# Kernel tuning notes

Measured on AMD Instinct MI355X. Metric: run time of the kernel, lower is better.

The kernel has to match this reference:

```python
import jax, jax.numpy as jnp
import numpy as np

B, T, C = 2, 2048, 2048
N_HEAD, N_KV = 16, 4
HD = C // N_HEAD          # 128
ROPE_THETA = 10000.0


def setup_inputs() -> dict:
    key = jax.random.key(0)
    ks = jax.random.split(key, 6)
    std = 0.02
    x = jax.random.normal(ks[0], (B, T, C), dtype=jnp.float32)
    Wq = jax.random.normal(ks[1], (C, C), dtype=jnp.float32) * std
    Wk = jax.random.normal(ks[2], (C, N_KV * HD), dtype=jnp.float32) * std
    Wv = jax.random.normal(ks[3], (C, N_KV * HD), dtype=jnp.float32) * std
    Wo = jax.random.normal(ks[4], (C, C), dtype=jnp.float32) * std
    # real RoPE frequencies: freqs_cis = exp(i * t * theta^{-2j/hd})
    inv_freq = 1.0 / (ROPE_THETA ** (jnp.arange(0, HD, 2, dtype=jnp.float32) / HD))
    ang = jnp.arange(T, dtype=jnp.float32)[:, None] * inv_freq[None, :]  # [T, HD//2]
    return {"x": x, "Wq": Wq, "Wk": Wk, "Wv": Wv, "Wo": Wo,
            "freqs_cos": jnp.cos(ang), "freqs_sin": jnp.sin(ang)}


def _rope(t, cos, sin):
    # t: [B, H, T, HD]; cos/sin: [T, HD//2] -> complex rotate even/odd pairs
    tr = t.reshape(*t.shape[:-1], HD // 2, 2)
    re, im = tr[..., 0], tr[..., 1]
    c = cos[None, None, :, :]
    s = sin[None, None, :, :]
    out = jnp.stack([re * c - im * s, re * s + im * c], axis=-1)
    return out.reshape(t.shape)


def reference(x, Wq, Wk, Wv, Wo, freqs_cos, freqs_sin):
    Bm, Tm, Cm = x.shape
    q = (x @ Wq).reshape(Bm, Tm, N_HEAD, HD).transpose(0, 2, 1, 3)  # [B,H,T,HD]
    k = (x @ Wk).reshape(Bm, Tm, N_KV, HD).transpose(0, 2, 1, 3)    # [B,Hkv,T,HD]
    v = (x @ Wv).reshape(Bm, Tm, N_KV, HD).transpose(0, 2, 1, 3)
    q = _rope(q, freqs_cos, freqs_sin)
    k = _rope(k, freqs_cos, freqs_sin)
    rep = N_HEAD // N_KV
    k = jnp.repeat(k, rep, axis=1)  # GQA repeat_kv -> [B,H,T,HD]
    v = jnp.repeat(v, rep, axis=1)
    scale = 1.0 / jnp.sqrt(jnp.asarray(HD, dtype=x.dtype))
    att = jnp.einsum("bhqd,bhkd->bhqk", q, k) * scale
    causal = jnp.tril(jnp.ones((Tm, Tm), dtype=bool))
    att = jnp.where(causal[None, None], att, jnp.asarray(-jnp.inf, att.dtype))
    att = jax.nn.softmax(att, axis=-1)
    y = jnp.einsum("bhqk,bhkd->bhqd", att, v)
    y = y.transpose(0, 2, 1, 3).reshape(Bm, Tm, Cm)
    return y @ Wo
```

## Files before the change

kernel.cpp:

```cpp
#include <hip/hip_runtime.h>

#define B_ 2
#define T_ 2048
#define C_ 2048
#define NH_ 16
#define NKV_ 4
#define HD_ 128
#define REP_ (NH_ / NKV_)
#define LDQKV 3072

typedef unsigned short u16;
typedef __bf16 bf16x8v __attribute__((ext_vector_type(8)));
typedef float f32x4v __attribute__((ext_vector_type(4)));

__device__ __forceinline__ u16 f2bf(float f) {
    unsigned int u;
    __builtin_memcpy(&u, &f, 4);
    u += 0x7FFFu + ((u >> 16) & 1u);
    return (u16)(u >> 16);
}
__device__ __forceinline__ unsigned int pk2(float a, float b) {
    unsigned int ua, ub;
    __builtin_memcpy(&ua, &a, 4);
    __builtin_memcpy(&ub, &b, 4);
    ua += 0x8000u; ub += 0x8000u;
    return (ua >> 16) | (ub & 0xFFFF0000u);
}
__device__ __forceinline__ bf16x8v load8(const u16* p) {
    return *reinterpret_cast<const bf16x8v*>(p);
}
__device__ __forceinline__ void gl16(const u16* g, u16* l) {
    __builtin_amdgcn_global_load_lds(
        (const __attribute__((address_space(1))) void*)(g),
        (__attribute__((address_space(3))) void*)(l), 16, 0, 0);
}
__device__ __forceinline__ void stg(const u16* g, u16* l, int tid, int K) {
    gl16(g, l + tid * 8);
    gl16(g + (size_t)64 * K, l + 4096 + tid * 8);
}
#define BAR()      __builtin_amdgcn_s_barrier()
#define LGKM0()    asm volatile("s_waitcnt lgkmcnt(0)" ::: "memory")
#define SCHED0()   __builtin_amdgcn_sched_barrier(0)
#define PRIO(x)    __builtin_amdgcn_s_setprio(x)

__global__ void cvt_f32_bf16(const float* __restrict__ in, u16* __restrict__ out, int n4) {
    int i = blockIdx.x * blockDim.x + threadIdx.x;
    if (i >= n4) return;
    float4 v = reinterpret_cast<const float4*>(in)[i];
    ushort4 o;
    o.x = f2bf(v.x); o.y = f2bf(v.y); o.z = f2bf(v.z); o.w = f2bf(v.w);
    reinterpret_cast<ushort4*>(out)[i] = o;
}

__global__ void xpose_f32_bf16(const float* __restrict__ in, u16* __restrict__ out,
                               int R, int Cc) {
    __shared__ u16 tile[32][33];
    int bx = blockIdx.x * 32, by = blockIdx.y * 32;
    int tx = threadIdx.x, ty = threadIdx.y;
    for (int i = 0; i < 32; i += 8)
        tile[ty + i][tx] = f2bf(in[(size_t)(by + ty + i) * Cc + bx + tx]);
    __syncthreads();
    for (int i = 0; i < 32; i += 8)
        out[(size_t)(bx + ty + i) * R + by + tx] = tile[tx][ty + i];
}

__global__ __launch_bounds__(512, 2) void gemm_qkv(const u16* __restrict__ A,
                                                   const u16* __restrict__ BT,
                                                   u16* __restrict__ Cq,
                                                   u16* __restrict__ vtb,
                                                   const float* __restrict__ cb,
                                                   const float* __restrict__ sb,
                                                   int M, int N, int K) {
    __shared__ __align__(16) u16 As[2][2][8192];
    __shared__ __align__(16) u16 Bs[2][2][8192];
    int tid = threadIdx.x;
    int lane = tid & 63, wave = tid >> 6;
    int wm = wave >> 2, wn = wave & 3;
    int m15 = lane & 15, quad = lane >> 4;

    int nbx = N >> 8;
    int bid = blockIdx.x, cpx = gridDim.x >> 3;
    int swz = (bid & 7) * cpx + (bid >> 3);
    int m0 = (swz / nbx) * 256, n0 = (swz % nbx) * 256;

    const u16* gA0 = A + (size_t)(m0 + (tid >> 3)) * K + (((tid & 7) ^ ((tid >> 3) & 7)) * 8);
    const u16* gB0 = BT + (size_t)(n0 + (tid >> 3)) * K + (((tid & 7) ^ ((tid >> 3) & 7)) * 8);

    int sw8 = m15 & 7;
    int co0 = (quad ^ sw8) * 8;
    int co1 = ((4 + quad) ^ sw8) * 8;
    const u16* aB = &As[0][0][0] + wm * 8192 + m15 * 64;
    const u16* bB = &Bs[0][0][0] + (wn >> 1) * 8192 + ((wn & 1) * 64 + m15) * 64;

    f32x4v acc[8][4] = {};
    int NT = K >> 6;

    stg(gB0, &Bs[0][0][0], tid, K);
    stg(gB0 + (size_t)128 * K, &Bs[0][1][0], tid, K);
    stg(gA0, &As[0][0][0], tid, K);
    stg(gA0 + (size_t)128 * K, &As[0][1][0], tid, K);
    stg(gB0 + 64, &Bs[1][0][0], tid, K);
    stg(gB0 + (size_t)128 * K + 64, &Bs[1][1][0], tid, K);
    asm volatile("s_waitcnt vmcnt(4)" ::: "memory");
    SCHED0();
    BAR();

    for (int t = 0; t < NT; t++) {
        int d = t & 1;
        const u16* aT = aB + d * 16384;
        const u16* bT = bB + d * 16384;
        bf16x8v a0[4][2], a1[4][2], b0[2][2], b1[2][2];

#pragma unroll
        for (int mt = 0; mt < 4; mt++) {
            a0[mt][0] = load8(aT + mt * 1024 + co0);
            a0[mt][1] = load8(aT + mt * 1024 + co1);
        }
#pragma unroll
        for (int nt = 0; nt < 2; nt++) {
            b0[nt][0] = load8(bT + nt * 1024 + co0);
            b0[nt][1] = load8(bT + nt * 1024 + co1);
        }
        if (t + 1 < NT) stg(gA0 + (t + 1) * 64, &As[1 - d][0][0], tid, K);
        BAR(); LGKM0(); SCHED0(); PRIO(1);
#pragma unroll
        for (int kc = 0; kc < 2; kc++)
#pragma unroll
            for (int mt = 0; mt < 4; mt++)
#pragma unroll
                for (int nt = 0; nt < 2; nt++)
                    acc[mt][nt] = __builtin_amdgcn_mfma_f32_16x16x32_bf16(
                        a0[mt][kc], b0[nt][kc], acc[mt][nt], 0, 0, 0);
        PRIO(0); BAR();

#pragma unroll
        for (int nt = 0; nt < 2; nt++) {
            b1[nt][0] = load8(bT + (nt + 2) * 1024 + co0);
            b1[nt][1] = load8(bT + (nt + 2) * 1024 + co1);
        }
        if (t + 1 < NT) stg(gA0 + (size_t)128 * K + (t + 1) * 64, &As[1 - d][1][0], tid, K);
        BAR(); LGKM0(); SCHED0(); PRIO(1);
#pragma unroll
        for (int kc = 0; kc < 2; kc++)
#pragma unroll
            for (int mt = 0; mt < 4; mt++)
#pragma unroll
                for (int nt = 0; nt < 2; nt++)
                    acc[mt][nt + 2] = __builtin_amdgcn_mfma_f32_16x16x32_bf16(
                        a0[mt][kc], b1[nt][kc], acc[mt][nt + 2], 0, 0, 0);
        PRIO(0); BAR();

#pragma unroll
        for (int mt = 0; mt < 4; mt++) {
            a1[mt][0] = load8(aT + (mt + 4) * 1024 + co0);
            a1[mt][1] = load8(aT + (mt + 4) * 1024 + co1);
        }
        if (t + 2 < NT) stg(gB0 + (t + 2) * 64, &Bs[d][0][0], tid, K);
        BAR(); LGKM0(); SCHED0(); PRIO(1);
#pragma unroll
        for (int kc = 0; kc < 2; kc++)
#pragma unroll
            for (int mt = 0; mt < 4; mt++)
#pragma unroll
                for (int nt = 0; nt < 2; nt++)
                    acc[mt + 4][nt] = __builtin_amdgcn_mfma_f32_16x16x32_bf16(
                        a1[mt][kc], b0[nt][kc], acc[mt + 4][nt], 0, 0, 0);
        PRIO(0); BAR();

        if (t + 2 < NT) stg(gB0 + (size_t)128 * K + (t + 2) * 64, &Bs[d][1][0], tid, K);
        BAR(); PRIO(1);
#pragma unroll
        for (int kc = 0; kc < 2; kc++)
#pragma unroll
            for (int mt = 0; mt < 4; mt++)
#pragma unroll
                for (int nt = 0; nt < 2; nt++)
                    acc[mt + 4][nt + 2] = __builtin_amdgcn_mfma_f32_16x16x32_bf16(
                        a1[mt][kc], b1[nt][kc], acc[mt + 4][nt + 2], 0, 0, 0);
        PRIO(0);
        if (t + 2 < NT) { asm volatile("s_waitcnt vmcnt(4)" ::: "memory"); }
        else            { asm volatile("s_waitcnt vmcnt(0)" ::: "memory"); }
        SCHED0();
        BAR();
    }

    if (n0 >= 2560) {
#pragma unroll
        for (int mt = 0; mt < 8; mt++)
#pragma unroll
            for (int nt = 0; nt < 4; nt++) {
                int hd = n0 + wn * 64 + nt * 16 + m15 - 2560;
                int mbase = m0 + wm * 128 + mt * 16 + quad * 4;
                int bb = mbase >> 11, tok = mbase & 2047;
                int g = (tok & 31) >> 2;
                int off = (tok & ~31) + ((g & 3) * 8 + (g >> 2) * 4);
                ushort4 pk;
                pk.x = f2bf(acc[mt][nt][0]);
                pk.y = f2bf(acc[mt][nt][1]);
                pk.z = f2bf(acc[mt][nt][2]);
                pk.w = f2bf(acc[mt][nt][3]);
                *reinterpret_cast<ushort4*>(vtb + ((size_t)bb * 512 + hd) * T_ + off) = pk;
            }
    } else {
#pragma unroll
        for (int mt = 0; mt < 8; mt++)
#pragma unroll
            for (int nt = 0; nt < 4; nt++) {
                int c = n0 + wn * 64 + nt * 16 + m15;
                int i = (c & 127) >> 1;
                float sgn = (c & 1) ? 1.f : -1.f;
#pragma unroll
                for (int r = 0; r < 4; r++) {
                    int mrow = m0 + wm * 128 + mt * 16 + quad * 4 + r;
                    int tok = mrow & 2047;
                    float cv = cb[tok * 64 + i];
                    float sv = sb[tok * 64 + i];
                    float v = acc[mt][nt][r];
                    float pval = __shfl_xor(v, 1, 64);
                    float outv = fmaf(v, cv, pval * sv * sgn);
                    Cq[(size_t)mrow * N + c] = f2bf(outv);
                }
            }
    }
}

__global__ __launch_bounds__(512, 2) void gemm_out(const u16* __restrict__ A,
                                                   const u16* __restrict__ BT,
                                                   float* __restrict__ C,
                                                   int M, int N, int K) {
    __shared__ __align__(16) u16 As2[2][8192];
    __shared__ __align__(16) u16 Bs2[2][2][8192];
    int tid = threadIdx.x;
    int lane = tid & 63, wave = tid >> 6;
    int wm = wave >> 2, wn = wave & 3;
    int m15 = lane & 15, quad = lane >> 4;

    int nbx = N >> 8;
    int bid = blockIdx.x, cpx = gridDim.x >> 3;
    int swz = (bid & 7) * cpx + (bid >> 3);
    int m0 = (swz / nbx) * 128, n0 = (swz % nbx) * 256;

    const u16* gA0 = A + (size_t)(m0 + (tid >> 3)) * K + (((tid & 7) ^ ((tid >> 3) & 7)) * 8);
    const u16* gB0 = BT + (size_t)(n0 + (tid >> 3)) * K + (((tid & 7) ^ ((tid >> 3) & 7)) * 8);

    int sw8 = m15 & 7;
    int co0 = (quad ^ sw8) * 8;
    int co1 = ((4 + quad) ^ sw8) * 8;
    const u16* aB = &As2[0][0] + (wm * 64 + m15) * 64;
    const u16* bB = &Bs2[0][0][0] + (wn >> 1) * 8192 + ((wn & 1) * 64 + m15) * 64;

    f32x4v acc[4][4] = {};
    int NT = K >> 6;

    stg(gB0, &Bs2[0][0][0], tid, K);
    stg(gB0 + (size_t)128 * K, &Bs2[0][1][0], tid, K);
    stg(gA0, &As2[0][0], tid, K);
    stg(gB0 + 64, &Bs2[1][0][0], tid, K);
    stg(gB0 + (size_t)128 * K + 64, &Bs2[1][1][0], tid, K);
    asm volatile("s_waitcnt vmcnt(4)" ::: "memory");
    SCHED0();
    BAR();

    for (int t = 0; t < NT; t++) {
        int d = t & 1;
        const u16* aT = aB + d * 8192;
        const u16* bT = bB + d * 16384;
        bf16x8v a0[2][2], a1[2][2], b0[2][2], b1[2][2];

#pragma unroll
        for (int mt = 0; mt < 2; mt++) {
            a0[mt][0] = load8(aT + mt * 1024 + co0);
            a0[mt][1] = load8(aT + mt * 1024 + co1);
        }
#pragma unroll
        for (int nt = 0; nt < 2; nt++) {
            b0[nt][0] = load8(bT + nt * 1024 + co0);
            b0[nt][1] = load8(bT + nt * 1024 + co1);
        }
        if (t + 1 < NT) stg(gA0 + (t + 1) * 64, &As2[1 - d][0], tid, K);
        BAR(); LGKM0(); SCHED0(); PRIO(1);
#pragma unroll
        for (int kc = 0; kc < 2; kc++)
#pragma unroll
            for (int mt = 0; mt < 2; mt++)
#pragma unroll
                for (int nt = 0; nt < 2; nt++)
                    acc[mt][nt] = __builtin_amdgcn_mfma_f32_16x16x32_bf16(
                        a0[mt][kc], b0[nt][kc], acc[mt][nt], 0, 0, 0);
        PRIO(0); BAR();

#pragma unroll
        for (int nt = 0; nt < 2; nt++) {
            b1[nt][0] = load8(bT + (nt + 2) * 1024 + co0);
            b1[nt][1] = load8(bT + (nt + 2) * 1024 + co1);
        }
        BAR(); LGKM0(); SCHED0(); PRIO(1);
#pragma unroll
        for (int kc = 0; kc < 2; kc++)
#pragma unroll
            for (int mt = 0; mt < 2; mt++)
#pragma unroll
                for (int nt = 0; nt < 2; nt++)
                    acc[mt][nt + 2] = __builtin_amdgcn_mfma_f32_16x16x32_bf16(
                        a0[mt][kc], b1[nt][kc], acc[mt][nt + 2], 0, 0, 0);
        PRIO(0); BAR();

#pragma unroll
        for (int mt = 0; mt < 2; mt++) {
            a1[mt][0] = load8(aT + (mt + 2) * 1024 + co0);
            a1[mt][1] = load8(aT + (mt + 2) * 1024 + co1);
        }
        if (t + 2 < NT) stg(gB0 + (t + 2) * 64, &Bs2[d][0][0], tid, K);
        BAR(); LGKM0(); SCHED0(); PRIO(1);
#pragma unroll
        for (int kc = 0; kc < 2; kc++)
#pragma unroll
            for (int mt = 0; mt < 2; mt++)
#pragma unroll
                for (int nt = 0; nt < 2; nt++)
                    acc[mt + 2][nt] = __builtin_amdgcn_mfma_f32_16x16x32_bf16(
                        a1[mt][kc], b0[nt][kc], acc[mt + 2][nt], 0, 0, 0);
        PRIO(0); BAR();

        if (t + 2 < NT) stg(gB0 + (size_t)128 * K + (t + 2) * 64, &Bs2[d][1][0], tid, K);
        BAR(); PRIO(1);
#pragma unroll
        for (int kc = 0; kc < 2; kc++)
#pragma unroll
            for (int mt = 0; mt < 2; mt++)
#pragma unroll
                for (int nt = 0; nt < 2; nt++)
                    acc[mt + 2][nt + 2] = __builtin_amdgcn_mfma_f32_16x16x32_bf16(
                        a1[mt][kc], b1[nt][kc], acc[mt + 2][nt + 2], 0, 0, 0);
        PRIO(0);
        if (t + 2 < NT) { asm volatile("s_waitcnt vmcnt(4)" ::: "memory"); }
        else            { asm volatile("s_waitcnt vmcnt(0)" ::: "memory"); }
        SCHED0();
        BAR();
    }

#pragma unroll
    for (int mt = 0; mt < 4; mt++)
#pragma unroll
        for (int nt = 0; nt < 4; nt++) {
            int c = n0 + wn * 64 + nt * 16 + m15;
#pragma unroll
            for (int r = 0; r < 4; r++) {
                int mrow = m0 + wm * 64 + mt * 16 + quad * 4 + r;
                C[(size_t)mrow * N + c] = acc[mt][nt][r];
            }
        }
}

__device__ __forceinline__ void stage_k128(const u16* kB, u16* Kl, int kt, int tid) {
    int keyc = tid >> 4, ch = tid & 15;
    const u16* g = kB + (size_t)(kt + keyc) * LDQKV + (ch ^ keyc) * 8;
    u16* l = Kl + tid * 8;
    for (int j = 0; j < 8; j++) {
        gl16(g, l);
        g += (size_t)16 * LDQKV;
        l += 2048;
    }
}
__device__ __forceinline__ void stage_v128(const u16* vB, u16* Vl, int kt, int tid) {
    int hdc = tid >> 4, ch = tid & 15;
    const u16* g = vB + (size_t)hdc * T_ + kt + (ch ^ hdc) * 8;
    u16* l = Vl + tid * 8;
    for (int j = 0; j < 8; j++) {
        gl16(g, l);
        g += (size_t)16 * T_;
        l += 2048;
    }
}

__global__ __launch_bounds__(256) void flash_k(const u16* __restrict__ qkv,
                                               const u16* __restrict__ vtb,
                                               u16* __restrict__ yb) {
    __shared__ __align__(16) u16 Kl[128 * 128];
    __shared__ __align__(16) u16 Vl[128 * 128];
    int h = blockIdx.y, b = blockIdx.z;
    int kv = h / REP_;
    int tid = threadIdx.x;
    int lane = tid & 63, wave = tid >> 6;
    int m15 = lane & 15, quad = lane >> 4;
    const u16* kB = qkv + (size_t)b * T_ * LDQKV + 2048 + kv * HD_;
    const u16* vB = vtb + ((size_t)(b * NKV_ + kv)) * HD_ * T_;
    const float scale2 = 0.1275173723f;
    const float M0b = 8.0f;
    const float NEG = -3.0e38f;

    for (int p = 0; p < 2; p++) {
        int qt = (p == 0) ? (int)blockIdx.x : (31 - (int)blockIdx.x);
        int qt0 = qt * 64;
        int qrow = qt0 + wave * 16;
        int q_i = qrow + m15;
        const u16* qp = qkv + (size_t)(b * T_ + q_i) * LDQKV + h * HD_ + quad * 8;
        bf16x8v qf[4];
        for (int kc = 0; kc < 4; kc++) qf[kc] = load8(qp + kc * 32);
        f32x4v o[8] = {};
        f32x4v lacc = {};

        int iters = qt0 / 128 + 1;
        for (int it = 0; it < iters; it++) {
            int kt = it * 128;
            __syncthreads();
            stage_k128(kB, Kl, kt, tid);
            stage_v128(vB, Vl, kt, tid);
            __syncthreads();
            f32x4v s4[8];
            for (int nt = 0; nt < 8; nt++) s4[nt] = (f32x4v){0.f, 0.f, 0.f, 0.f};
            for (int nt = 0; nt < 8; nt++) {
                const u16* kls = Kl + (nt * 16 + m15) * 128;
                for (int kc = 0; kc < 4; kc++)
                    s4[nt] = __builtin_amdgcn_mfma_f32_16x16x32_bf16(
                        load8(kls + (((kc * 4 + quad) ^ m15) * 8)), qf[kc], s4[nt], 0, 0, 0);
            }
            if (kt + 128 > qt0) {
                for (int nt = 0; nt < 8; nt++) {
                    int key = kt + nt * 16 + quad * 4;
                    for (int r = 0; r < 4; r++)
                        if (key + r > q_i) s4[nt][r] = NEG;
                }
            }
            for (int nt = 0; nt < 8; nt++) {
                for (int r = 0; r < 4; r++)
                    s4[nt][r] = exp2f(fmaf(s4[nt][r], scale2, -M0b));
                lacc += s4[nt];
            }
            for (int c = 0; c < 4; c++) {
                unsigned int w[4];
                w[0] = pk2(s4[2 * c][0], s4[2 * c][1]);
                w[1] = pk2(s4[2 * c][2], s4[2 * c][3]);
                w[2] = pk2(s4[2 * c + 1][0], s4[2 * c + 1][1]);
                w[3] = pk2(s4[2 * c + 1][2], s4[2 * c + 1][3]);
                bf16x8v pf;
                __builtin_memcpy(&pf, w, 16);
                for (int dt = 0; dt < 8; dt++) {
                    const u16* vls = Vl + (dt * 16 + m15) * 128;
                    o[dt] = __builtin_amdgcn_mfma_f32_16x16x32_bf16(
                        load8(vls + (((c * 4 + quad) ^ m15) * 8)), pf, o[dt], 0, 0, 0);
                }
            }
        }
        float l = lacc[0] + lacc[1] + lacc[2] + lacc[3];
        l += __shfl_xor(l, 16, 64);
        l += __shfl_xor(l, 32, 64);
        float inv = 1.f / l;
        u16* yp = yb + (size_t)(b * T_ + q_i) * C_ + h * HD_ + quad * 4;
        for (int dt = 0; dt < 8; dt++) {
            ushort4 pk;
            pk.x = f2bf(o[dt][0] * inv);
            pk.y = f2bf(o[dt][1] * inv);
            pk.z = f2bf(o[dt][2] * inv);
            pk.w = f2bf(o[dt][3] * inv);
            *reinterpret_cast<ushort4*>(yp + dt * 16) = pk;
        }
    }
}

extern "C" void kernel_launch(void* const* d_in, const int* in_sizes, int n_in,
                              void* d_out, int out_size, void* d_ws, size_t ws_size,
                              hipStream_t stream) {
    const float* x  = (const float*)d_in[0];
    const float* Wq = (const float*)d_in[1];
    const float* Wk = (const float*)d_in[2];
    const float* Wv = (const float*)d_in[3];
    const float* Wo = (const float*)d_in[4];
    const float* fc = (const float*)d_in[5];
    const float* fs = (const float*)d_in[6];
    float* out = (float*)d_out;

    char* ws = (char*)d_ws;
    u16* WqkvT = (u16*)(ws);
    u16* WoT   = (u16*)(ws + 12582912);
    u16* xb    = (u16*)(ws + 20971520);
    u16* qkvb  = (u16*)(ws + 37748736);
    u16* vtb   = (u16*)(ws + 62914560);
    u16* yb    = (u16*)(ws + 67108864);

    const int M = B_ * T_;

    int n4 = (M * C_) / 4;
    cvt_f32_bf16<<<n4 / 256, 256, 0, stream>>>(x, xb, n4);

    dim3 tb(32, 8);
    xpose_f32_bf16<<<dim3(C_ / 32, C_ / 32), tb, 0, stream>>>(Wq, WqkvT, C_, C_);
    xpose_f32_bf16<<<dim3((NKV_ * HD_) / 32, C_ / 32), tb, 0, stream>>>(Wk, WqkvT + 2048 * 2048, C_, NKV_ * HD_);
    xpose_f32_bf16<<<dim3((NKV_ * HD_) / 32, C_ / 32), tb, 0, stream>>>(Wv, WqkvT + 2560 * 2048, C_, NKV_ * HD_);
    xpose_f32_bf16<<<dim3(C_ / 32, C_ / 32), tb, 0, stream>>>(Wo, WoT, C_, C_);

    gemm_qkv<<<dim3((LDQKV / 256) * (M / 256)), 512, 0, stream>>>(xb, WqkvT, qkvb, vtb, fc, fs, M, LDQKV, C_);

    flash_k<<<dim3(T_ / 128, NH_, B_), 256, 0, stream>>>(qkvb, vtb, yb);

    gemm_out<<<dim3((C_ / 256) * (M / 128)), 512, 0, stream>>>(yb, WoT, out, M, C_, C_);
}
```

Baseline: 297.6 us.

## Retile QKV GEMM to 256x192 and double-buffer flash attention KV tiles

The QKV projection GEMM moves from 256x256 to 256x192 tiles, giving 256 blocks instead of 192 for better CU coverage on the 3072-wide output, with B staged as three 64-row slabs. The V-transpose epilogue is merged into a per-column branch. The flash attention kernel switches from synchronous single-buffered 128-key tiles to double-buffered 64-key K/V tiles. It prefetches the next tile with async global-to-LDS loads while running MFMAs, to hide load latency behind compute. This adds more barriers per iteration and a finer-grained pipeline whose vmcnt bookkeeping must stay correct.

```diff
diff --git a/kernel.cpp b/kernel.cpp
--- a/kernel.cpp
+++ b/kernel.cpp
@@ -37,6 +37,11 @@
 __device__ __forceinline__ void stg(const u16* g, u16* l, int tid, int K) {
     gl16(g, l + tid * 8);
     gl16(g + (size_t)64 * K, l + 4096 + tid * 8);
+}
+__device__ __forceinline__ void stgB3(const u16* g, u16* l, int tid, int K) {
+    gl16(g, l + tid * 8);
+    gl16(g + (size_t)64 * K, l + 4096 + tid * 8);
+    gl16(g + (size_t)128 * K, l + 8192 + tid * 8);
 }
 #define BAR()      __builtin_amdgcn_s_barrier()
 #define LGKM0()    asm volatile("s_waitcnt lgkmcnt(0)" ::: "memory")
@@ -72,44 +77,43 @@
                                                    const float* __restrict__ sb,
                                                    int M, int N, int K) {
     __shared__ __align__(16) u16 As[2][2][8192];
-    __shared__ __align__(16) u16 Bs[2][2][8192];
+    __shared__ __align__(16) u16 Bs[2][12288];
     int tid = threadIdx.x;
     int lane = tid & 63, wave = tid >> 6;
     int wm = wave >> 2, wn = wave & 3;
     int m15 = lane & 15, quad = lane >> 4;
 
-    int nbx = N >> 8;
+    int nbx = N / 192;
     int bid = blockIdx.x, cpx = gridDim.x >> 3;
     int swz = (bid & 7) * cpx + (bid >> 3);
-    int m0 = (swz / nbx) * 256, n0 = (swz % nbx) * 256;
-
-    const u16* gA0 = A + (size_t)(m0 + (tid >> 3)) * K + (((tid & 7) ^ ((tid >> 3) & 7)) * 8);
-    const u16* gB0 = BT + (size_t)(n0 + (tid >> 3)) * K + (((tid & 7) ^ ((tid >> 3) & 7)) * 8);
+    int m0 = (swz / nbx) * 256, n0 = (swz % nbx) * 192;
+
+    int r_ = tid >> 3, c_ = tid & 7;
+    const u16* gA0 = A + (size_t)(m0 + r_) * K + ((c_ ^ (r_ & 7)) * 8);
+    const u16* gB0 = BT + (size_t)(n0 + r_) * K + ((c_ ^ (r_ & 7)) * 8);
 
     int sw8 = m15 & 7;
     int co0 = (quad ^ sw8) * 8;
     int co1 = ((4 + quad) ^ sw8) * 8;
     const u16* aB = &As[0][0][0] + wm * 8192 + m15 * 64;
-    const u16* bB = &Bs[0][0][0] + (wn >> 1) * 8192 + ((wn & 1) * 64 + m15) * 64;
-
-    f32x4v acc[8][4] = {};
+    const u16* bB = &Bs[0][0] + (wn * 48 + m15) * 64;
+
+    f32x4v acc[8][3] = {};
     int NT = K >> 6;
 
-    stg(gB0, &Bs[0][0][0], tid, K);
-    stg(gB0 + (size_t)128 * K, &Bs[0][1][0], tid, K);
+    stgB3(gB0, &Bs[0][0], tid, K);
     stg(gA0, &As[0][0][0], tid, K);
     stg(gA0 + (size_t)128 * K, &As[0][1][0], tid, K);
-    stg(gB0 + 64, &Bs[1][0][0], tid, K);
-    stg(gB0 + (size_t)128 * K + 64, &Bs[1][1][0], tid, K);
-    asm volatile("s_waitcnt vmcnt(4)" ::: "memory");
+    stgB3(gB0 + 64, &Bs[1][0], tid, K);
+    asm volatile("s_waitcnt vmcnt(3)" ::: "memory");
     SCHED0();
     BAR();
 
     for (int t = 0; t < NT; t++) {
         int d = t & 1;
         const u16* aT = aB + d * 16384;
-        const u16* bT = bB + d * 16384;
-        bf16x8v a0[4][2], a1[4][2], b0[2][2], b1[2][2];
+        const u16* bT = bB + d * 12288;
+        bf16x8v a0[4][2], a1[4][2], bv[3][2];
 
 #pragma unroll
         for (int mt = 0; mt < 4; mt++) {
@@ -118,8 +122,8 @@
         }
 #pragma unroll
         for (int nt = 0; nt < 2; nt++) {
-            b0[nt][0] = load8(bT + nt * 1024 + co0);
-            b0[nt][1] = load8(bT + nt * 1024 + co1);
+            bv[nt][0] = load8(bT + nt * 1024 + co0);
+            bv[nt][1] = load8(bT + nt * 1024 + co1);
         }
         if (t + 1 < NT) stg(gA0 + (t + 1) * 64, &As[1 - d][0][0], tid, K);
         BAR(); LGKM0(); SCHED0(); PRIO(1);
@@ -130,24 +134,7 @@
 #pragma unroll
                 for (int nt = 0; nt < 2; nt++)
                     acc[mt][nt] = __builtin_amdgcn_mfma_f32_16x16x32_bf16(
-                        a0[mt][kc], b0[nt][kc], acc[mt][nt], 0, 0, 0);
-        PRIO(0); BAR();
-
-#pragma unroll
-        for (int nt = 0; nt < 2; nt++) {
-            b1[nt][0] = load8(bT + (nt + 2) * 1024 + co0);
-            b1[nt][1] = load8(bT + (nt + 2) * 1024 + co1);
-        }
-        if (t + 1 < NT) stg(gA0 + (size_t)128 * K + (t + 1) * 64, &As[1 - d][1][0], tid, K);
-        BAR(); LGKM0(); SCHED0(); PRIO(1);
-#pragma unroll
-        for (int kc = 0; kc < 2; kc++)
-#pragma unroll
-            for (int mt = 0; mt < 4; mt++)
-#pragma unroll
-                for (int nt = 0; nt < 2; nt++)
-                    acc[mt][nt + 2] = __builtin_amdgcn_mfma_f32_16x16x32_bf16(
-                        a0[mt][kc], b1[nt][kc], acc[mt][nt + 2], 0, 0, 0);
+                        a0[mt][kc], bv[nt][kc], acc[mt][nt], 0, 0, 0);
         PRIO(0); BAR();
 
 #pragma unroll
@@ -155,7 +142,9 @@
             a1[mt][0] = load8(aT + (mt + 4) * 1024 + co0);
             a1[mt][1] = load8(aT + (mt + 4) * 1024 + co1);
         }
-        if (t + 2 < NT) stg(gB0 + (t + 2) * 64, &Bs[d][0][0], tid, K);
+        bv[2][0] = load8(bT + 2048 + co0);
+        bv[2][1] = load8(bT + 2048 + co1);
+        if (t + 1 < NT) stg(gA0 + (size_t)128 * K + (t + 1) * 64, &As[1 - d][1][0], tid, K);
         BAR(); LGKM0(); SCHED0(); PRIO(1);
 #pragma unroll
         for (int kc = 0; kc < 2; kc++)
@@ -164,32 +153,37 @@
 #pragma unroll
                 for (int nt = 0; nt < 2; nt++)
                     acc[mt + 4][nt] = __builtin_amdgcn_mfma_f32_16x16x32_bf16(
-                        a1[mt][kc], b0[nt][kc], acc[mt + 4][nt], 0, 0, 0);
+                        a1[mt][kc], bv[nt][kc], acc[mt + 4][nt], 0, 0, 0);
         PRIO(0); BAR();
 
-        if (t + 2 < NT) stg(gB0 + (size_t)128 * K + (t + 2) * 64, &Bs[d][1][0], tid, K);
-        BAR(); PRIO(1);
+        if (t + 2 < NT) stgB3(gB0 + (t + 2) * 64, &Bs[d][0], tid, K);
+        PRIO(1);
 #pragma unroll
         for (int kc = 0; kc < 2; kc++)
 #pragma unroll
             for (int mt = 0; mt < 4; mt++)
-#pragma unroll
-                for (int nt = 0; nt < 2; nt++)
-                    acc[mt + 4][nt + 2] = __builtin_amdgcn_mfma_f32_16x16x32_bf16(
-                        a1[mt][kc], b1[nt][kc], acc[mt + 4][nt + 2], 0, 0, 0);
+                acc[mt][2] = __builtin_amdgcn_mfma_f32_16x16x32_bf16(
+                    a0[mt][kc], bv[2][kc], acc[mt][2], 0, 0, 0);
+#pragma unroll
+        for (int kc = 0; kc < 2; kc++)
+#pragma unroll
+            for (int mt = 0; mt < 4; mt++)
+                acc[mt + 4][2] = __builtin_amdgcn_mfma_f32_16x16x32_bf16(
+                    a1[mt][kc], bv[2][kc], acc[mt + 4][2], 0, 0, 0);
         PRIO(0);
-        if (t + 2 < NT) { asm volatile("s_waitcnt vmcnt(4)" ::: "memory"); }
+        if (t + 2 < NT) { asm volatile("s_waitcnt vmcnt(3)" ::: "memory"); }
         else            { asm volatile("s_waitcnt vmcnt(0)" ::: "memory"); }
         SCHED0();
         BAR();
     }
 
-    if (n0 >= 2560) {
-#pragma unroll
-        for (int mt = 0; mt < 8; mt++)
-#pragma unroll
-            for (int nt = 0; nt < 4; nt++) {
-                int hd = n0 + wn * 64 + nt * 16 + m15 - 2560;
+#pragma unroll
+    for (int mt = 0; mt < 8; mt++)
+#pragma unroll
+        for (int nt = 0; nt < 3; nt++) {
+            int c = n0 + wn * 48 + nt * 16 + m15;
+            if (c >= 2560) {
+                int hd = c - 2560;
                 int mbase = m0 + wm * 128 + mt * 16 + quad * 4;
                 int bb = mbase >> 11, tok = mbase & 2047;
                 int g = (tok & 31) >> 2;
@@ -200,13 +194,7 @@
                 pk.z = f2bf(acc[mt][nt][2]);
                 pk.w = f2bf(acc[mt][nt][3]);
                 *reinterpret_cast<ushort4*>(vtb + ((size_t)bb * 512 + hd) * T_ + off) = pk;
-            }
-    } else {
-#pragma unroll
-        for (int mt = 0; mt < 8; mt++)
-#pragma unroll
-            for (int nt = 0; nt < 4; nt++) {
-                int c = n0 + wn * 64 + nt * 16 + m15;
+            } else {
                 int i = (c & 127) >> 1;
                 float sgn = (c & 1) ? 1.f : -1.f;
 #pragma unroll
@@ -221,7 +209,7 @@
                     Cq[(size_t)mrow * N + c] = f2bf(outv);
                 }
             }
-    }
+        }
 }
 
 __global__ __launch_bounds__(512, 2) void gemm_out(const u16* __restrict__ A,
@@ -352,23 +340,25 @@
         }
 }
 
-__device__ __forceinline__ void stage_k128(const u16* kB, u16* Kl, int kt, int tid) {
+__device__ __forceinline__ void stgK64(const u16* kB, u16* Kl, int kt, int tid) {
     int keyc = tid >> 4, ch = tid & 15;
     const u16* g = kB + (size_t)(kt + keyc) * LDQKV + (ch ^ keyc) * 8;
     u16* l = Kl + tid * 8;
-    for (int j = 0; j < 8; j++) {
+#pragma unroll
+    for (int j = 0; j < 4; j++) {
         gl16(g, l);
         g += (size_t)16 * LDQKV;
         l += 2048;
     }
 }
-__device__ __forceinline__ void stage_v128(const u16* vB, u16* Vl, int kt, int tid) {
-    int hdc = tid >> 4, ch = tid & 15;
-    const u16* g = vB + (size_t)hdc * T_ + kt + (ch ^ hdc) * 8;
+__device__ __forceinline__ void stgV64(const u16* vB, u16* Vl, int kt, int tid) {
+    int hdc = tid >> 3, ch = tid & 7;
+    const u16* g = vB + (size_t)hdc * T_ + kt + (ch ^ (hdc & 7)) * 8;
     u16* l = Vl + tid * 8;
-    for (int j = 0; j < 8; j++) {
+#pragma unroll
+    for (int j = 0; j < 4; j++) {
         gl16(g, l);
-        g += (size_t)16 * T_;
+        g += (size_t)32 * T_;
         l += 2048;
     }
 }
@@ -376,13 +366,14 @@
 __global__ __launch_bounds__(256) void flash_k(const u16* __restrict__ qkv,
                                                const u16* __restrict__ vtb,
                                                u16* __restrict__ yb) {
-    __shared__ __align__(16) u16 Kl[128 * 128];
-    __shared__ __align__(16) u16 Vl[128 * 128];
+    __shared__ __align__(16) u16 Kl[2][64 * 128];
+    __shared__ __align__(16) u16 Vl[2][128 * 64];
     int h = blockIdx.y, b = blockIdx.z;
     int kv = h / REP_;
     int tid = threadIdx.x;
     int lane = tid & 63, wave = tid >> 6;
     int m15 = lane & 15, quad = lane >> 4;
+    int sw8 = m15 & 7;
     const u16* kB = qkv + (size_t)b * T_ * LDQKV + 2048 + kv * HD_;
     const u16* vB = vtb + ((size_t)(b * NKV_ + kv)) * HD_ * T_;
     const float scale2 = 0.1275173723f;
@@ -392,61 +383,102 @@
     for (int p = 0; p < 2; p++) {
         int qt = (p == 0) ? (int)blockIdx.x : (31 - (int)blockIdx.x);
         int qt0 = qt * 64;
-        int qrow = qt0 + wave * 16;
-        int q_i = qrow + m15;
+        int q_i = qt0 + wave * 16 + m15;
         const u16* qp = qkv + (size_t)(b * T_ + q_i) * LDQKV + h * HD_ + quad * 8;
         bf16x8v qf[4];
+#pragma unroll
         for (int kc = 0; kc < 4; kc++) qf[kc] = load8(qp + kc * 32);
         f32x4v o[8] = {};
         f32x4v lacc = {};
-
-        int iters = qt0 / 128 + 1;
-        for (int it = 0; it < iters; it++) {
-            int kt = it * 128;
-            __syncthreads();
-            stage_k128(kB, Kl, kt, tid);
-            stage_v128(vB, Vl, kt, tid);
-            __syncthreads();
-            f32x4v s4[8];
-            for (int nt = 0; nt < 8; nt++) s4[nt] = (f32x4v){0.f, 0.f, 0.f, 0.f};
-            for (int nt = 0; nt < 8; nt++) {
-                const u16* kls = Kl + (nt * 16 + m15) * 128;
+        int NT = qt + 1;
+
+        stgK64(kB, &Kl[0][0], 0, tid);
+        stgV64(vB, &Vl[0][0], 0, tid);
+        stgK64(kB, &Kl[1][0], 64, tid);
+        stgV64(vB, &Vl[1][0], 64, tid);
+        asm volatile("s_waitcnt vmcnt(8)" ::: "memory");
+        SCHED0();
+        BAR();
+
+        for (int it = 0; it < NT; it++) {
+            int cur = it & 1;
+            int kt = it * 64;
+            const u16* Kc = &Kl[cur][0];
+            const u16* Vc = &Vl[cur][0];
+
+            bf16x8v kf[4][4];
+#pragma unroll
+            for (int nt = 0; nt < 4; nt++) {
+                const u16* kls = Kc + (nt * 16 + m15) * 128;
+#pragma unroll
+                for (int kc = 0; kc < 4; kc++)
+                    kf[nt][kc] = load8(kls + (((kc * 4 + quad) ^ m15) * 8));
+            }
+            if (it >= 1 && it + 1 < NT) stgK64(kB, &Kl[1 - cur][0], kt + 64, tid);
+            BAR(); LGKM0(); SCHED0(); PRIO(1);
+            f32x4v s4[4] = {};
+#pragma unroll
+            for (int nt = 0; nt < 4; nt++)
+#pragma unroll
                 for (int kc = 0; kc < 4; kc++)
                     s4[nt] = __builtin_amdgcn_mfma_f32_16x16x32_bf16(
-                        load8(kls + (((kc * 4 + quad) ^ m15) * 8)), qf[kc], s4[nt], 0, 0, 0);
-            }
-            if (kt + 128 > qt0) {
-                for (int nt = 0; nt < 8; nt++) {
+                        kf[nt][kc], qf[kc], s4[nt], 0, 0, 0);
+            PRIO(0);
+            if (it + 1 < NT) { asm volatile("s_waitcnt vmcnt(4)" ::: "memory"); }
+            else             { asm volatile("s_waitcnt vmcnt(0)" ::: "memory"); }
+            SCHED0(); BAR();
+
+            if (kt + 64 > qt0) {
+#pragma unroll
+                for (int nt = 0; nt < 4; nt++) {
                     int key = kt + nt * 16 + quad * 4;
+#pragma unroll
                     for (int r = 0; r < 4; r++)
                         if (key + r > q_i) s4[nt][r] = NEG;
                 }
             }
-            for (int nt = 0; nt < 8; nt++) {
+#pragma unroll
+            for (int nt = 0; nt < 4; nt++) {
+#pragma unroll
                 for (int r = 0; r < 4; r++)
                     s4[nt][r] = exp2f(fmaf(s4[nt][r], scale2, -M0b));
                 lacc += s4[nt];
             }
-            for (int c = 0; c < 4; c++) {
+            bf16x8v pf[2];
+#pragma unroll
+            for (int c = 0; c < 2; c++) {
                 unsigned int w[4];
                 w[0] = pk2(s4[2 * c][0], s4[2 * c][1]);
                 w[1] = pk2(s4[2 * c][2], s4[2 * c][3]);
                 w[2] = pk2(s4[2 * c + 1][0], s4[2 * c + 1][1]);
                 w[3] = pk2(s4[2 * c + 1][2], s4[2 * c + 1][3]);
-                bf16x8v pf;
-                __builtin_memcpy(&pf, w, 16);
-                for (int dt = 0; dt < 8; dt++) {
-                    const u16* vls = Vl + (dt * 16 + m15) * 128;
+                __builtin_memcpy(&pf[c], w, 16);
+            }
+            bf16x8v vf[2][8];
+#pragma unroll
+            for (int c = 0; c < 2; c++)
+#pragma unroll
+                for (int dt = 0; dt < 8; dt++)
+                    vf[c][dt] = load8(Vc + (dt * 16 + m15) * 64 + (((c * 4 + quad) ^ sw8) * 8));
+            if (it >= 1 && it + 1 < NT) stgV64(vB, &Vl[1 - cur][0], kt + 64, tid);
+            BAR(); LGKM0(); SCHED0(); PRIO(1);
+#pragma unroll
+            for (int c = 0; c < 2; c++)
+#pragma unroll
+                for (int dt = 0; dt < 8; dt++)
                     o[dt] = __builtin_amdgcn_mfma_f32_16x16x32_bf16(
-                        load8(vls + (((c * 4 + quad) ^ m15) * 8)), pf, o[dt], 0, 0, 0);
-                }
-            }
-        }
+                        vf[c][dt], pf[c], o[dt], 0, 0, 0);
+            PRIO(0);
+            if (it + 1 < NT) { asm volatile("s_waitcnt vmcnt(4)" ::: "memory"); }
+            SCHED0(); BAR();
+        }
+
         float l = lacc[0] + lacc[1] + lacc[2] + lacc[3];
         l += __shfl_xor(l, 16, 64);
         l += __shfl_xor(l, 32, 64);
         float inv = 1.f / l;
         u16* yp = yb + (size_t)(b * T_ + q_i) * C_ + h * HD_ + quad * 4;
+#pragma unroll
         for (int dt = 0; dt < 8; dt++) {
             ushort4 pk;
             pk.x = f2bf(o[dt][0] * inv);
@@ -489,7 +521,7 @@
     xpose_f32_bf16<<<dim3((NKV_ * HD_) / 32, C_ / 32), tb, 0, stream>>>(Wv, WqkvT + 2560 * 2048, C_, NKV_ * HD_);
     xpose_f32_bf16<<<dim3(C_ / 32, C_ / 32), tb, 0, stream>>>(Wo, WoT, C_, C_);
 
-    gemm_qkv<<<dim3((LDQKV / 256) * (M / 256)), 512, 0, stream>>>(xb, WqkvT, qkvb, vtb, fc, fs, M, LDQKV, C_);
+    gemm_qkv<<<dim3((LDQKV / 192) * (M / 256)), 512, 0, stream>>>(xb, WqkvT, qkvb, vtb, fc, fs, M, LDQKV, C_);
 
     flash_k<<<dim3(T_ / 128, NH_, B_), 256, 0, stream>>>(qkvb, vtb, yb);
 
```

Result: faster. 289.7 us (-2.7%).
